# Optimization experiments

Hardware: AMD Instinct MI355X
Metric: run time of the kernel (lower is better)

## Reference

```python
import jax, jax.numpy as jnp
import numpy as np

RADIUS = 0.1
K = 32  # num_neighbors


def _ball_query(points, centers, radius, k):
    # points: [B,3,N], centers: [B,3,M] -> indices [B,M,K] (int32)
    # PVCNN semantics: first k point indices within radius of each center,
    # unfilled slots padded with the first in-ball index (0 if none in ball).
    N = points.shape[-1]
    p2 = jnp.sum(points * points, axis=1)            # [B,N]
    c2 = jnp.sum(centers * centers, axis=1)          # [B,M]
    cp = jnp.einsum('bdm,bdn->bmn', centers, points)  # [B,M,N]
    dist2 = c2[:, :, None] + p2[:, None, :] - 2.0 * cp
    valid = dist2 < radius * radius                  # [B,M,N]
    # score = point index if in ball else sentinel N; sorting ascending puts
    # the first k in-ball indices (in original point order) up front.
    scores = jnp.where(valid, jnp.arange(N, dtype=jnp.int32), jnp.int32(N))
    idx = jnp.sort(scores, axis=-1)[..., :k]         # [B,M,K]
    first = idx[..., :1]
    first = jnp.where(first == N, 0, first)          # no neighbor -> index 0
    return jnp.where(idx == N, first, idx)


def _group(feat, idx):
    # feat: [B,C,N], idx: [B,M,K] -> [B,C,M,K]
    return jnp.take_along_axis(feat[:, :, None, :], idx[:, None, :, :], axis=3)


def setup_inputs() -> dict:
    key = jax.random.key(0)
    k1, k2, k3 = jax.random.split(key, 3)
    B, N, M, C = 2, 16384, 4096, 32
    points_coords = jax.random.uniform(k1, (B, 3, N), dtype=jnp.float32)
    centers_coords = jax.random.uniform(k2, (B, 3, M), dtype=jnp.float32)
    points_features = jax.random.normal(k3, (B, C, N), dtype=jnp.float32)
    return {
        'points_coords': points_coords,
        'centers_coords': centers_coords,
        'points_features': points_features,
    }


def reference(points_coords, centers_coords, points_features):
    idx = _ball_query(points_coords, centers_coords, RADIUS, K)     # [B,M,K]
    nbr_coords = _group(points_coords, idx)                          # [B,3,M,K]
    nbr_coords = nbr_coords - centers_coords[:, :, :, None]         # relative
    nbr_feats = _group(points_features, idx)                         # [B,C,M,K]
    out = jnp.concatenate([nbr_coords, nbr_feats], axis=1)          # [B,3+C,M,K]
    return jnp.transpose(out, (0, 1, 3, 2))                          # [B,3+C,K,M]
```

## Files before the change

### kernel.cpp

```cpp
#include <hip/hip_runtime.h>

#define B_SZ  2
#define N_PTS 16384
#define M_CTR 4096
#define C_FT  32
#define K_NB  32
#define NCH   35
#define CH_STRIDE (K_NB * M_CTR)
#define CELLS 10
#define NCELL (CELLS * CELLS * CELLS)

__device__ __forceinline__ float fmul(float a, float b) {
    float r; asm("v_mul_f32 %0, %1, %2" : "=v"(r) : "v"(a), "v"(b)); return r;
}
__device__ __forceinline__ float fadd(float a, float b) {
    float r; asm("v_add_f32 %0, %1, %2" : "=v"(r) : "v"(a), "v"(b)); return r;
}
__device__ __forceinline__ float fsub(float a, float b) {
    float r; asm("v_sub_f32 %0, %1, %2" : "=v"(r) : "v"(a), "v"(b)); return r;
}
__device__ __forceinline__ float ffma(float a, float b, float c) {
    float r; asm("v_fma_f32 %0, %1, %2, %3" : "=v"(r) : "v"(a), "v"(b), "v"(c));
    return r;
}

__device__ __forceinline__ bool bq_valid(float x, float y, float z,
                                         float cx, float cy, float cz,
                                         float c2, float r2) {
    const float p2 = fadd(fadd(fmul(x, x), fmul(y, y)), fmul(z, z));
    const float cp = ffma(cz, z, ffma(cy, y, fmul(cx, x)));
    return fsub(fadd(c2, p2), fmul(2.0f, cp)) < r2;
}

__device__ __forceinline__ int cell_of(float x, float y, float z) {
    int ci = (int)(x * 10.0f); ci = ci < 0 ? 0 : (ci > 9 ? 9 : ci);
    int cj = (int)(y * 10.0f); cj = cj < 0 ? 0 : (cj > 9 ? 9 : cj);
    int ck = (int)(z * 10.0f); ck = ck < 0 ? 0 : (ck > 9 ? 9 : ck);
    return (ck * CELLS + cj) * CELLS + ci;
}

__global__ __launch_bounds__(256) void zero_kernel(int* __restrict__ hist) {
    const int t = blockIdx.x * 256 + threadIdx.x;
    if (t < B_SZ * NCELL) hist[t] = 0;
}

__global__ __launch_bounds__(256) void hist_kernel(
    const float* __restrict__ points, int* __restrict__ hist) {
    const int t = blockIdx.x * 256 + threadIdx.x;
    const int b = t >> 14, n = t & (N_PTS - 1);
    const float x = points[(b * 3 + 0) * N_PTS + n];
    const float y = points[(b * 3 + 1) * N_PTS + n];
    const float z = points[(b * 3 + 2) * N_PTS + n];
    atomicAdd(&hist[b * NCELL + cell_of(x, y, z)], 1);
}

__global__ __launch_bounds__(1024) void scan_kernel(
    const int* __restrict__ hist, int* __restrict__ starts,
    int* __restrict__ cursor) {
    __shared__ int s[1024];
    const int t = threadIdx.x;
    for (int b = 0; b < B_SZ; ++b) {
        s[t] = (t < NCELL) ? hist[b * NCELL + t] : 0;
        __syncthreads();
        for (int off = 1; off < 1024; off <<= 1) {
            const int v = (t >= off) ? s[t - off] : 0;
            __syncthreads();
            s[t] += v;
            __syncthreads();
        }
        if (t < NCELL) {
            const int st = (t == 0) ? 0 : s[t - 1];
            starts[b * (NCELL + 1) + t] = st;
            cursor[b * NCELL + t] = st;
        }
        if (t == 0) starts[b * (NCELL + 1) + NCELL] = s[NCELL - 1];
        __syncthreads();
    }
}

__global__ __launch_bounds__(256) void scatter_kernel(
    const float* __restrict__ points, int* __restrict__ cursor,
    float4* __restrict__ binned) {
    const int t = blockIdx.x * 256 + threadIdx.x;
    const int b = t >> 14, n = t & (N_PTS - 1);
    const float x = points[(b * 3 + 0) * N_PTS + n];
    const float y = points[(b * 3 + 1) * N_PTS + n];
    const float z = points[(b * 3 + 2) * N_PTS + n];
    const int pos = atomicAdd(&cursor[b * NCELL + cell_of(x, y, z)], 1);
    binned[b * N_PTS + pos] = make_float4(x, y, z, __int_as_float(n));
}

__global__ __launch_bounds__(256) void ball_query_kernel(
    const float4* __restrict__ binned,
    const float* __restrict__ centers,
    const int* __restrict__ starts,
    int* __restrict__ idx_out)
{
    const int lane = threadIdx.x & 63;
    const int wid  = threadIdx.x >> 6;
    const int cid  = blockIdx.x * 4 + wid;
    const int b = cid >> 12;
    const int m = cid & (M_CTR - 1);

    const float r2 = (float)(0.1 * 0.1);

    const float cx = centers[(b * 3 + 0) * M_CTR + m];
    const float cy = centers[(b * 3 + 1) * M_CTR + m];
    const float cz = centers[(b * 3 + 2) * M_CTR + m];
    const float c2 = fadd(fadd(fmul(cx, cx), fmul(cy, cy)), fmul(cz, cz));

    __shared__ unsigned bitmap[4][N_PTS / 32];
    unsigned* bm = bitmap[wid];
#pragma unroll
    for (int j = 0; j < 8; ++j) bm[lane * 8 + j] = 0u;

    int ci = (int)(cx * 10.0f); ci = ci < 0 ? 0 : (ci > 9 ? 9 : ci);
    int cj = (int)(cy * 10.0f); cj = cj < 0 ? 0 : (cj > 9 ? 9 : cj);
    int ck = (int)(cz * 10.0f); ck = ck < 0 ? 0 : (ck > 9 ? 9 : ck);
    const int i0 = ci > 0 ? ci - 1 : 0;
    const int i1 = ci < 9 ? ci + 1 : 9;
    const int* st = starts + b * (NCELL + 1);
    const float4* __restrict__ bp = binned + b * N_PTS;

    for (int d = 0; d < 9; ++d) {
        const int jj = cj + (d % 3) - 1;
        const int kk = ck + (d / 3) - 1;
        if (jj < 0 || jj > 9 || kk < 0 || kk > 9) continue;
        const int base = (kk * CELLS + jj) * CELLS;
        const int lo = st[base + i0];
        const int hi = st[base + i1 + 1];
        for (int s0 = lo; s0 < hi; s0 += 64) {
            const int t = s0 + lane;
            if (t < hi) {
                const float4 p = bp[t];
                if (bq_valid(p.x, p.y, p.z, cx, cy, cz, c2, r2)) {
                    const int n = __float_as_int(p.w);
                    atomicOr((int*)&bm[n >> 5], 1 << (n & 31));
                }
            }
        }
    }

    unsigned w[8];
    int cnt = 0;
#pragma unroll
    for (int j = 0; j < 8; ++j) { w[j] = bm[lane * 8 + j]; cnt += __popc(w[j]); }

    int incl = cnt;
    for (int off = 1; off < 64; off <<= 1) {
        const int v = __shfl_up(incl, off);
        if (lane >= off) incl += v;
    }
    const int total = __shfl(incl, 63);
    int slot = incl - cnt;

    int firstbit = 0x7fffffff;
#pragma unroll
    for (int j = 0; j < 8; ++j) {
        if (w[j] && firstbit == 0x7fffffff)
            firstbit = lane * 256 + j * 32 + (__ffs(w[j]) - 1);
    }
    for (int off = 32; off > 0; off >>= 1)
        firstbit = min(firstbit, __shfl_xor(firstbit, off));
    const int first_idx = (total == 0) ? 0 : firstbit;

    int* __restrict__ dst = idx_out + (b * K_NB) * M_CTR + m;
#pragma unroll
    for (int j = 0; j < 8; ++j) {
        unsigned x = w[j];
        while (x && slot < K_NB) {
            const int bit = __ffs(x) - 1;
            dst[slot * M_CTR] = lane * 256 + j * 32 + bit;
            x &= x - 1;
            ++slot;
        }
    }
    if (lane >= total && lane < K_NB) dst[lane * M_CTR] = first_idx;
}

__global__ __launch_bounds__(256) void transpose_kernel(
    const float* __restrict__ points,
    const float* __restrict__ feats,
    float* __restrict__ pf)
{
    __shared__ float tile[64][37];
    const int t  = threadIdx.x;
    const int b  = blockIdx.x >> 8;
    const int n0 = (blockIdx.x & 255) * 64;

    for (int i = t; i < NCH * 64; i += 256) {
        const int r = i >> 6;
        const int c = i & 63;
        float v;
        if (r < 3) v = points[(b * 3 + r) * N_PTS + n0 + c];
        else       v = feats[(b * C_FT + (r - 3)) * N_PTS + n0 + c];
        tile[c][r] = v;
    }
    if (t < 64) tile[t][35] = 0.0f;
    __syncthreads();

    float* __restrict__ dst = pf + ((size_t)b * N_PTS + n0) * 36;
    for (int o = t; o < 64 * 36; o += 256) {
        const int c = o / 36;
        const int r = o - c * 36;
        dst[o] = tile[c][r];
    }
}

__global__ __launch_bounds__(256) void gather_kernel(
    const float* __restrict__ pf,
    const float* __restrict__ centers,
    const int* __restrict__ idx,
    float* __restrict__ out)
{
    const int t = blockIdx.x * 256 + threadIdx.x;
    const int m = t & (M_CTR - 1);
    const int k = (t >> 12) & (K_NB - 1);
    const int b = t >> 17;

    const int n = idx[(b * K_NB + k) * M_CTR + m];
    const float4* __restrict__ src = (const float4*)(pf + ((size_t)b * N_PTS + n) * 36);

    float4 f[9];
#pragma unroll
    for (int i = 0; i < 9; ++i) f[i] = src[i];

    const float cx = centers[(b * 3 + 0) * M_CTR + m];
    const float cy = centers[(b * 3 + 1) * M_CTR + m];
    const float cz = centers[(b * 3 + 2) * M_CTR + m];

    float vv[36];
#pragma unroll
    for (int i = 0; i < 9; ++i) {
        vv[4 * i + 0] = f[i].x; vv[4 * i + 1] = f[i].y;
        vv[4 * i + 2] = f[i].z; vv[4 * i + 3] = f[i].w;
    }
    vv[0] -= cx; vv[1] -= cy; vv[2] -= cz;

    float* __restrict__ o = out + ((size_t)b * NCH * K_NB + k) * M_CTR + m;
#pragma unroll
    for (int ch = 0; ch < NCH; ++ch)
        o[(size_t)ch * CH_STRIDE] = vv[ch];
}

extern "C" void kernel_launch(void* const* d_in, const int* in_sizes, int n_in,
                              void* d_out, int out_size, void* d_ws, size_t ws_size,
                              hipStream_t stream) {
    const float* points  = (const float*)d_in[0];
    const float* centers = (const float*)d_in[1];
    const float* feats   = (const float*)d_in[2];
    float* out = (float*)d_out;

    char* ws = (char*)d_ws;
    int*    idx    = (int*)ws;
    float*  pf     = (float*)(ws + (1u << 20));
    int*    hist   = (int*)(ws + 5700 * 1024);
    int*    cursor = (int*)(ws + 5716 * 1024);
    int*    starts = (int*)(ws + 5732 * 1024);
    float4* binned = (float4*)(ws + 5764 * 1024);

    zero_kernel<<<(B_SZ * NCELL + 255) / 256, 256, 0, stream>>>(hist);
    hist_kernel<<<(B_SZ * N_PTS) / 256, 256, 0, stream>>>(points, hist);
    scan_kernel<<<1, 1024, 0, stream>>>(hist, starts, cursor);
    scatter_kernel<<<(B_SZ * N_PTS) / 256, 256, 0, stream>>>(points, cursor, binned);
    transpose_kernel<<<B_SZ * (N_PTS / 64), 256, 0, stream>>>(points, feats, pf);

    ball_query_kernel<<<(B_SZ * M_CTR) / 4, 256, 0, stream>>>(
        binned, centers, starts, idx);

    const int total = B_SZ * K_NB * M_CTR;
    gather_kernel<<<total / 256, 256, 0, stream>>>(pf, centers, idx, out);
}
```

Baseline: 114.5 us.

## Fuse scatter and transpose, warp-shuffle scan, memset hist, two centers per gather thread

```diff
diff --git a/kernel.cpp b/kernel.cpp
--- a/kernel.cpp
+++ b/kernel.cpp
@@ -39,11 +39,6 @@
     return (ck * CELLS + cj) * CELLS + ci;
 }
 
-__global__ __launch_bounds__(256) void zero_kernel(int* __restrict__ hist) {
-    const int t = blockIdx.x * 256 + threadIdx.x;
-    if (t < B_SZ * NCELL) hist[t] = 0;
-}
-
 __global__ __launch_bounds__(256) void hist_kernel(
     const float* __restrict__ points, int* __restrict__ hist) {
     const int t = blockIdx.x * 256 + threadIdx.x;
@@ -57,37 +52,71 @@
 __global__ __launch_bounds__(1024) void scan_kernel(
     const int* __restrict__ hist, int* __restrict__ starts,
     int* __restrict__ cursor) {
-    __shared__ int s[1024];
+    const int b = blockIdx.x;
     const int t = threadIdx.x;
-    for (int b = 0; b < B_SZ; ++b) {
-        s[t] = (t < NCELL) ? hist[b * NCELL + t] : 0;
+    const int lane = t & 63, wid = t >> 6;
+    __shared__ int wsum[16];
+    const int v = (t < NCELL) ? hist[b * NCELL + t] : 0;
+    int incl = v;
+    for (int off = 1; off < 64; off <<= 1) {
+        const int u = __shfl_up(incl, off);
+        if (lane >= off) incl += u;
+    }
+    if (lane == 63) wsum[wid] = incl;
+    __syncthreads();
+    if (wid == 0 && lane < 16) {
+        const int s = wsum[lane];
+        int in2 = s;
+        for (int off = 1; off < 16; off <<= 1) {
+            const int u = __shfl_up(in2, off);
+            if (lane >= off) in2 += u;
+        }
+        wsum[lane] = in2 - s;
+    }
+    __syncthreads();
+    if (t < NCELL) {
+        const int excl = incl - v + wsum[wid];
+        starts[b * (NCELL + 1) + t] = excl;
+        cursor[b * NCELL + t] = excl;
+        if (t == NCELL - 1) starts[b * (NCELL + 1) + NCELL] = excl + v;
+    }
+}
+
+__global__ __launch_bounds__(256) void scatter_transpose_kernel(
+    const float* __restrict__ points, const float* __restrict__ feats,
+    int* __restrict__ cursor, float4* __restrict__ binned,
+    float* __restrict__ pf) {
+    if (blockIdx.x < 128) {
+        const int t = blockIdx.x * 256 + threadIdx.x;
+        const int b = t >> 14, n = t & (N_PTS - 1);
+        const float x = points[(b * 3 + 0) * N_PTS + n];
+        const float y = points[(b * 3 + 1) * N_PTS + n];
+        const float z = points[(b * 3 + 2) * N_PTS + n];
+        const int pos = atomicAdd(&cursor[b * NCELL + cell_of(x, y, z)], 1);
+        binned[b * N_PTS + pos] = make_float4(x, y, z, __int_as_float(n));
+    } else {
+        __shared__ float tile[64][37];
+        const int bid = blockIdx.x - 128;
+        const int t  = threadIdx.x;
+        const int b  = bid >> 8;
+        const int n0 = (bid & 255) * 64;
+        for (int i = t; i < NCH * 64; i += 256) {
+            const int r = i >> 6;
+            const int c = i & 63;
+            float v;
+            if (r < 3) v = points[(b * 3 + r) * N_PTS + n0 + c];
+            else       v = feats[(b * C_FT + (r - 3)) * N_PTS + n0 + c];
+            tile[c][r] = v;
+        }
+        if (t < 64) tile[t][35] = 0.0f;
         __syncthreads();
-        for (int off = 1; off < 1024; off <<= 1) {
-            const int v = (t >= off) ? s[t - off] : 0;
-            __syncthreads();
-            s[t] += v;
-            __syncthreads();
-        }
-        if (t < NCELL) {
-            const int st = (t == 0) ? 0 : s[t - 1];
-            starts[b * (NCELL + 1) + t] = st;
-            cursor[b * NCELL + t] = st;
-        }
-        if (t == 0) starts[b * (NCELL + 1) + NCELL] = s[NCELL - 1];
-        __syncthreads();
-    }
-}
-
-__global__ __launch_bounds__(256) void scatter_kernel(
-    const float* __restrict__ points, int* __restrict__ cursor,
-    float4* __restrict__ binned) {
-    const int t = blockIdx.x * 256 + threadIdx.x;
-    const int b = t >> 14, n = t & (N_PTS - 1);
-    const float x = points[(b * 3 + 0) * N_PTS + n];
-    const float y = points[(b * 3 + 1) * N_PTS + n];
-    const float z = points[(b * 3 + 2) * N_PTS + n];
-    const int pos = atomicAdd(&cursor[b * NCELL + cell_of(x, y, z)], 1);
-    binned[b * N_PTS + pos] = make_float4(x, y, z, __int_as_float(n));
+        float* __restrict__ dst = pf + ((size_t)b * N_PTS + n0) * 36;
+        for (int o = t; o < 64 * 36; o += 256) {
+            const int c = o / 36;
+            const int r = o - c * 36;
+            dst[o] = tile[c][r];
+        }
+    }
 }
 
 __global__ __launch_bounds__(256) void ball_query_kernel(
@@ -178,35 +207,6 @@
     if (lane >= total && lane < K_NB) dst[lane * M_CTR] = first_idx;
 }
 
-__global__ __launch_bounds__(256) void transpose_kernel(
-    const float* __restrict__ points,
-    const float* __restrict__ feats,
-    float* __restrict__ pf)
-{
-    __shared__ float tile[64][37];
-    const int t  = threadIdx.x;
-    const int b  = blockIdx.x >> 8;
-    const int n0 = (blockIdx.x & 255) * 64;
-
-    for (int i = t; i < NCH * 64; i += 256) {
-        const int r = i >> 6;
-        const int c = i & 63;
-        float v;
-        if (r < 3) v = points[(b * 3 + r) * N_PTS + n0 + c];
-        else       v = feats[(b * C_FT + (r - 3)) * N_PTS + n0 + c];
-        tile[c][r] = v;
-    }
-    if (t < 64) tile[t][35] = 0.0f;
-    __syncthreads();
-
-    float* __restrict__ dst = pf + ((size_t)b * N_PTS + n0) * 36;
-    for (int o = t; o < 64 * 36; o += 256) {
-        const int c = o / 36;
-        const int r = o - c * 36;
-        dst[o] = tile[c][r];
-    }
-}
-
 __global__ __launch_bounds__(256) void gather_kernel(
     const float* __restrict__ pf,
     const float* __restrict__ centers,
@@ -214,33 +214,39 @@
     float* __restrict__ out)
 {
     const int t = blockIdx.x * 256 + threadIdx.x;
-    const int m = t & (M_CTR - 1);
-    const int k = (t >> 12) & (K_NB - 1);
-    const int b = t >> 17;
-
-    const int n = idx[(b * K_NB + k) * M_CTR + m];
-    const float4* __restrict__ src = (const float4*)(pf + ((size_t)b * N_PTS + n) * 36);
-
-    float4 f[9];
-#pragma unroll
-    for (int i = 0; i < 9; ++i) f[i] = src[i];
-
-    const float cx = centers[(b * 3 + 0) * M_CTR + m];
-    const float cy = centers[(b * 3 + 1) * M_CTR + m];
-    const float cz = centers[(b * 3 + 2) * M_CTR + m];
-
-    float vv[36];
+    const int m = (t & (M_CTR / 2 - 1)) * 2;
+    const int k = (t >> 11) & (K_NB - 1);
+    const int b = t >> 16;
+
+    const int2 nn = *(const int2*)&idx[(b * K_NB + k) * M_CTR + m];
+    const float4* __restrict__ s0 =
+        (const float4*)(pf + ((size_t)b * N_PTS + nn.x) * 36);
+    const float4* __restrict__ s1 =
+        (const float4*)(pf + ((size_t)b * N_PTS + nn.y) * 36);
+
+    float4 f0[9], f1[9];
+#pragma unroll
+    for (int i = 0; i < 9; ++i) { f0[i] = s0[i]; f1[i] = s1[i]; }
+
+    const float2 cx = *(const float2*)&centers[(b * 3 + 0) * M_CTR + m];
+    const float2 cy = *(const float2*)&centers[(b * 3 + 1) * M_CTR + m];
+    const float2 cz = *(const float2*)&centers[(b * 3 + 2) * M_CTR + m];
+
+    float v0[36], v1[36];
 #pragma unroll
     for (int i = 0; i < 9; ++i) {
-        vv[4 * i + 0] = f[i].x; vv[4 * i + 1] = f[i].y;
-        vv[4 * i + 2] = f[i].z; vv[4 * i + 3] = f[i].w;
-    }
-    vv[0] -= cx; vv[1] -= cy; vv[2] -= cz;
+        v0[4 * i + 0] = f0[i].x; v0[4 * i + 1] = f0[i].y;
+        v0[4 * i + 2] = f0[i].z; v0[4 * i + 3] = f0[i].w;
+        v1[4 * i + 0] = f1[i].x; v1[4 * i + 1] = f1[i].y;
+        v1[4 * i + 2] = f1[i].z; v1[4 * i + 3] = f1[i].w;
+    }
+    v0[0] -= cx.x; v0[1] -= cy.x; v0[2] -= cz.x;
+    v1[0] -= cx.y; v1[1] -= cy.y; v1[2] -= cz.y;
 
     float* __restrict__ o = out + ((size_t)b * NCH * K_NB + k) * M_CTR + m;
 #pragma unroll
     for (int ch = 0; ch < NCH; ++ch)
-        o[(size_t)ch * CH_STRIDE] = vv[ch];
+        *(float2*)&o[(size_t)ch * CH_STRIDE] = make_float2(v0[ch], v1[ch]);
 }
 
 extern "C" void kernel_launch(void* const* d_in, const int* in_sizes, int n_in,
@@ -259,15 +265,13 @@
     int*    starts = (int*)(ws + 5732 * 1024);
     float4* binned = (float4*)(ws + 5764 * 1024);
 
-    zero_kernel<<<(B_SZ * NCELL + 255) / 256, 256, 0, stream>>>(hist);
+    hipMemsetAsync(hist, 0, B_SZ * NCELL * sizeof(int), stream);
     hist_kernel<<<(B_SZ * N_PTS) / 256, 256, 0, stream>>>(points, hist);
-    scan_kernel<<<1, 1024, 0, stream>>>(hist, starts, cursor);
-    scatter_kernel<<<(B_SZ * N_PTS) / 256, 256, 0, stream>>>(points, cursor, binned);
-    transpose_kernel<<<B_SZ * (N_PTS / 64), 256, 0, stream>>>(points, feats, pf);
-
+    scan_kernel<<<B_SZ, 1024, 0, stream>>>(hist, starts, cursor);
+    scatter_transpose_kernel<<<128 + B_SZ * (N_PTS / 64), 256, 0, stream>>>(
+        points, feats, cursor, binned, pf);
     ball_query_kernel<<<(B_SZ * M_CTR) / 4, 256, 0, stream>>>(
         binned, centers, starts, idx);
-
-    const int total = B_SZ * K_NB * M_CTR;
-    gather_kernel<<<total / 256, 256, 0, stream>>>(pf, centers, idx, out);
-}
+    gather_kernel<<<(B_SZ * K_NB * M_CTR / 2) / 256, 256, 0, stream>>>(
+        pf, centers, idx, out);
+}
```

After: 108.6 us. -5.2%, faster.
